# Optimization experiments

Hardware: AMD Instinct MI355X
Metric: run time of the kernel (lower is better)

The kernel has to match this reference:

```python
import jax, jax.numpy as jnp
import numpy as np

H = 256  # rnn_size


def setup_inputs() -> dict:
    key = jax.random.key(0)
    ks = jax.random.split(key, 6)
    B, T, F, D = 64, 512, 64, 64
    s_in = 1.0 / np.sqrt(F)
    s_rec = 1.0 / np.sqrt(H)
    return {
        "x": jax.random.normal(ks[0], (B, T, F), jnp.float32),
        "kernel": jax.random.normal(ks[1], (F, 3 * H), jnp.float32) * s_in,
        "recurrent_kernel": jax.random.normal(ks[2], (H, 3 * H), jnp.float32) * s_rec,
        "bias": jax.random.normal(ks[3], (3 * H,), jnp.float32) * 0.01,
        "dense_w": jax.random.normal(ks[4], (H, D), jnp.float32) * s_rec,
        "dense_b": jax.random.normal(ks[5], (D,), jnp.float32) * 0.01,
    }


def _gru_scan(x, kernel, recurrent_kernel, bias):
    B, T, _ = x.shape
    # Pre-project all timesteps: [B, T, 3H]
    xproj = jnp.einsum("btf,fg->btg", x, kernel) + bias
    xproj_t = jnp.transpose(xproj, (1, 0, 2))  # [T, B, 3H]

    def step(h, xt):
        # Keras GRU, reset_after=False: r gates the recurrent matmul of the candidate
        rec = h @ recurrent_kernel  # [B, 3H]
        xz, xr, xh = xt[:, :H], xt[:, H:2 * H], xt[:, 2 * H:]
        rz, rr, rh = rec[:, :H], rec[:, H:2 * H], rec[:, 2 * H:]
        z = jax.nn.sigmoid(xz + rz)
        r = jax.nn.sigmoid(xr + rr)
        hh = jnp.tanh(xh + r * rh)
        h_new = z * h + (1.0 - z) * hh
        return h_new, h_new

    h0 = jnp.zeros((B, H), x.dtype)
    h_last, outs = jax.lax.scan(step, h0, xproj_t)
    return jnp.transpose(outs, (1, 0, 2)), h_last  # [B,T,H], [B,H]


def reference(x, kernel, recurrent_kernel, bias, dense_w, dense_b):
    outputs, h_last = _gru_scan(x, kernel, recurrent_kernel, bias)
    state = jnp.tanh(h_last @ dense_w + dense_b)  # [B, dense_size]
    return outputs, state
```

## Files before the change

### kernel.cpp

```cpp
#include <hip/hip_runtime.h>


typedef _Float16 half2_t __attribute__((ext_vector_type(2)));
typedef _Float16 f16x4_t __attribute__((ext_vector_type(4)));

#define LOG2E 1.4426950408889634f

__device__ __forceinline__ float fast_sigmoid(float x) {
  float e = __builtin_amdgcn_exp2f(-x * LOG2E);
  return __builtin_amdgcn_rcpf(1.0f + e);
}
__device__ __forceinline__ float fast_tanh(float x) {
  float e = __builtin_amdgcn_exp2f(x * (2.0f * LOG2E));
  return 1.0f - 2.0f * __builtin_amdgcn_rcpf(1.0f + e);
}

__global__ __launch_bounds__(256, 4) void xproj_gemm(
    const float* __restrict__ x, const float* __restrict__ kmat,
    const float* __restrict__ bias, _Float16* __restrict__ xp) {
  __shared__ half2_t As2[32][132];
  __shared__ half2_t Bs2[32][132];
  const int tid = threadIdx.x;
  const int rb = blockIdx.x * 128;
  const int cb = blockIdx.y * 128;

  {
    const int k4 = (tid & 15) * 4;
    const int r0 = tid >> 4;
#pragma unroll
    for (int p = 0; p < 8; ++p) {
      int r = r0 + p * 16;
      float4 v = *(const float4*)(x + (size_t)(rb + r) * 64 + k4);
      half2_t lo, hi;
      lo[0] = (_Float16)v.x; lo[1] = (_Float16)v.y;
      hi[0] = (_Float16)v.z; hi[1] = (_Float16)v.w;
      As2[k4 / 2][r] = lo;
      As2[k4 / 2 + 1][r] = hi;
    }
  }
  {
    const int c4 = (tid & 31) * 4;
    const int kp0 = tid >> 5;
#pragma unroll
    for (int p = 0; p < 4; ++p) {
      int kp = kp0 + p * 8;
      float4 va = *(const float4*)(kmat + (size_t)(2 * kp) * 768 + cb + c4);
      float4 vb = *(const float4*)(kmat + (size_t)(2 * kp + 1) * 768 + cb + c4);
      half2_t o0, o1, o2, o3;
      o0[0] = (_Float16)va.x; o0[1] = (_Float16)vb.x;
      o1[0] = (_Float16)va.y; o1[1] = (_Float16)vb.y;
      o2[0] = (_Float16)va.z; o2[1] = (_Float16)vb.z;
      o3[0] = (_Float16)va.w; o3[1] = (_Float16)vb.w;
      Bs2[kp][c4 + 0] = o0;
      Bs2[kp][c4 + 1] = o1;
      Bs2[kp][c4 + 2] = o2;
      Bs2[kp][c4 + 3] = o3;
    }
  }
  __syncthreads();

  const int tx = tid & 15, ty = tid >> 4;
  const int r0 = ty * 8;
  const int c0 = tx * 4;
  float acc[8][8];
  {
    float4 b0 = *(const float4*)(bias + cb + c0);
    float4 b1 = *(const float4*)(bias + cb + 64 + c0);
    float bz[8] = {b0.x, b0.y, b0.z, b0.w, b1.x, b1.y, b1.z, b1.w};
#pragma unroll
    for (int i = 0; i < 8; ++i)
#pragma unroll
      for (int j = 0; j < 8; ++j) acc[i][j] = bz[j];
  }

#pragma unroll 2
  for (int kp = 0; kp < 32; ++kp) {
    half2_t a2[8], b2[8];
    *(int4*)(&a2[0]) = *(const int4*)(&As2[kp][r0]);
    *(int4*)(&a2[4]) = *(const int4*)(&As2[kp][r0 + 4]);
    *(int2*)(&b2[0]) = *(const int2*)(&Bs2[kp][c0]);
    *(int2*)(&b2[2]) = *(const int2*)(&Bs2[kp][c0 + 2]);
    *(int2*)(&b2[4]) = *(const int2*)(&Bs2[kp][64 + c0]);
    *(int2*)(&b2[6]) = *(const int2*)(&Bs2[kp][64 + c0 + 2]);
#pragma unroll
    for (int i = 0; i < 8; ++i)
#pragma unroll
      for (int j = 0; j < 8; ++j)
        acc[i][j] = __builtin_amdgcn_fdot2(a2[i], b2[j], acc[i][j], false);
  }

#pragma unroll
  for (int i = 0; i < 8; ++i) {
    f16x4_t o0, o1;
#pragma unroll
    for (int j = 0; j < 4; ++j) {
      o0[j] = (_Float16)acc[i][j];
      o1[j] = (_Float16)acc[i][4 + j];
    }
    _Float16* dst = xp + (size_t)(rb + r0 + i) * 768 + cb;
    *(f16x4_t*)(dst + c0) = o0;
    *(f16x4_t*)(dst + 64 + c0) = o1;
  }
}

__global__ __launch_bounds__(512, 2) void gru_scan(
    const _Float16* __restrict__ xp, const float* __restrict__ wr,
    const float* __restrict__ dw, const float* __restrict__ db,
    float* __restrict__ out, float* __restrict__ state) {
  __shared__ float part[3 * 256];
  __shared__ float hbuf[256];
  __shared__ alignas(16) _Float16 hhalf[256];

  const int tid = threadIdx.x;
  const int b = blockIdx.x;
  const int c = tid >> 8;
  const int col = tid & 255;

  half2_t w2[3][64];
#pragma unroll
  for (int q = 0; q < 3; ++q) {
    const float* wp = wr + (size_t)(c * 128) * 768 + col + q * 256;
#pragma unroll
    for (int j = 0; j < 64; ++j) {
      float wa = wp[(size_t)(2 * j) * 768];
      float wb = wp[(size_t)(2 * j + 1) * 768];
      half2_t p;
      p[0] = (_Float16)wa;
      p[1] = (_Float16)wb;
      w2[q][j] = p;
    }
  }

  if (tid < 256) hhalf[tid] = (_Float16)0.0f;
  __syncthreads();

  const _Float16* xpb = xp + (size_t)b * 512 * 768;
  float* outb = out + (size_t)b * 512 * 256;
  const int4* hp = (const int4*)hhalf + c * 16;
  float hprev = 0.0f;

  for (int t = 0; t < 512; ++t) {
    float xz = 0.0f, xr = 0.0f, xh = 0.0f;
    if (tid < 256) {
      const _Float16* xr0 = xpb + (size_t)t * 768 + tid;
      xz = (float)xr0[0];
      xr = (float)xr0[256];
      xh = (float)xr0[512];
    }

    float a0 = 0.0f, a1 = 0.0f, a2 = 0.0f;
    int4 hv = hp[0];
#pragma unroll
    for (int g = 0; g < 16; ++g) {
      int4 hn = hv;
      if (g < 15) hn = hp[g + 1];
      half2_t p0 = __builtin_bit_cast(half2_t, hv.x);
      half2_t p1 = __builtin_bit_cast(half2_t, hv.y);
      half2_t p2 = __builtin_bit_cast(half2_t, hv.z);
      half2_t p3 = __builtin_bit_cast(half2_t, hv.w);
      a0 = __builtin_amdgcn_fdot2(p0, w2[0][g * 4 + 0], a0, false);
      a0 = __builtin_amdgcn_fdot2(p1, w2[0][g * 4 + 1], a0, false);
      a0 = __builtin_amdgcn_fdot2(p2, w2[0][g * 4 + 2], a0, false);
      a0 = __builtin_amdgcn_fdot2(p3, w2[0][g * 4 + 3], a0, false);
      a1 = __builtin_amdgcn_fdot2(p0, w2[1][g * 4 + 0], a1, false);
      a1 = __builtin_amdgcn_fdot2(p1, w2[1][g * 4 + 1], a1, false);
      a1 = __builtin_amdgcn_fdot2(p2, w2[1][g * 4 + 2], a1, false);
      a1 = __builtin_amdgcn_fdot2(p3, w2[1][g * 4 + 3], a1, false);
      a2 = __builtin_amdgcn_fdot2(p0, w2[2][g * 4 + 0], a2, false);
      a2 = __builtin_amdgcn_fdot2(p1, w2[2][g * 4 + 1], a2, false);
      a2 = __builtin_amdgcn_fdot2(p2, w2[2][g * 4 + 2], a2, false);
      a2 = __builtin_amdgcn_fdot2(p3, w2[2][g * 4 + 3], a2, false);
      hv = hn;
    }
    if (tid >= 256) {
      part[col] = a0;
      part[256 + col] = a1;
      part[512 + col] = a2;
    }
    __syncthreads();

    if (tid < 256) {
      const int i = tid;
      if (t) outb[(size_t)(t - 1) * 256 + i] = hprev;
      float rz = a0 + part[i];
      float rr = a1 + part[256 + i];
      float rh = a2 + part[512 + i];
      float z = fast_sigmoid(xz + rz);
      float r = fast_sigmoid(xr + rr);
      float hh = fast_tanh(xh + r * rh);
      float hnew = z * hprev + (1.0f - z) * hh;
      hprev = hnew;
      hhalf[i] = (_Float16)hnew;
    }
    __syncthreads();
  }

  if (tid < 256) {
    outb[(size_t)511 * 256 + tid] = hprev;
    hbuf[tid] = hprev;
  }
  __syncthreads();

  if (tid < 64) {
    float acc = db[tid];
#pragma unroll 8
    for (int k = 0; k < 256; ++k) acc = fmaf(hbuf[k], dw[k * 64 + tid], acc);
    state[(size_t)b * 64 + tid] = fast_tanh(acc);
  }
}

extern "C" void kernel_launch(void* const* d_in, const int* in_sizes, int n_in,
                              void* d_out, int out_size, void* d_ws,
                              size_t ws_size, hipStream_t stream) {
  const float* x = (const float*)d_in[0];
  const float* kmat = (const float*)d_in[1];
  const float* wr = (const float*)d_in[2];
  const float* bias = (const float*)d_in[3];
  const float* dw = (const float*)d_in[4];
  const float* db = (const float*)d_in[5];

  float* out = (float*)d_out;
  float* state = out + (size_t)64 * 512 * 256;
  _Float16* xp = (_Float16*)d_ws;

  dim3 gg(32768 / 128, 768 / 128);
  xproj_gemm<<<gg, 256, 0, stream>>>(x, kmat, bias, xp);
  gru_scan<<<64, 512, 0, stream>>>(xp, wr, dw, db, out, state);
}
```

Baseline: 707.5 us.

## Batch 16 sequences per block and compute GRU recurrence with MFMA

Replaces the per-sequence scan (one block per batch row, fdot2 reductions split over two halves plus a partial-sum exchange) with a block handling 16 batch rows. The recurrent matmul runs as 16x16x32 f16 MFMA with weight fragments held in registers, and h is double-buffered in LDS so each step needs only one barrier. This removes the second barrier and the partial-sum traffic per step and puts the matmul on matrix cores. The trade-off is that only 4 blocks run, so very few CUs are used and each step's latency is bounded by one block's MFMA chain plus scattered xp loads and output stores.

```diff
diff --git a/kernel.cpp b/kernel.cpp
--- a/kernel.cpp
+++ b/kernel.cpp
@@ -3,6 +3,8 @@
 
 typedef _Float16 half2_t __attribute__((ext_vector_type(2)));
 typedef _Float16 f16x4_t __attribute__((ext_vector_type(4)));
+typedef _Float16 f16x8_t __attribute__((ext_vector_type(8)));
+typedef float f32x4_t __attribute__((ext_vector_type(4)));
 
 #define LOG2E 1.4426950408889634f
 
@@ -103,109 +105,99 @@
   }
 }
 
-__global__ __launch_bounds__(512, 2) void gru_scan(
+__global__ __launch_bounds__(512, 1) void gru_scan_mfma(
     const _Float16* __restrict__ xp, const float* __restrict__ wr,
     const float* __restrict__ dw, const float* __restrict__ db,
     float* __restrict__ out, float* __restrict__ state) {
-  __shared__ float part[3 * 256];
-  __shared__ float hbuf[256];
-  __shared__ alignas(16) _Float16 hhalf[256];
+  __shared__ _Float16 hA[2][16][264];
+  __shared__ float hf[16][256];
 
   const int tid = threadIdx.x;
-  const int b = blockIdx.x;
-  const int c = tid >> 8;
-  const int col = tid & 255;
-
-  half2_t w2[3][64];
-#pragma unroll
-  for (int q = 0; q < 3; ++q) {
-    const float* wp = wr + (size_t)(c * 128) * 768 + col + q * 256;
-#pragma unroll
-    for (int j = 0; j < 64; ++j) {
-      float wa = wp[(size_t)(2 * j) * 768];
-      float wb = wp[(size_t)(2 * j + 1) * 768];
-      half2_t p;
-      p[0] = (_Float16)wa;
-      p[1] = (_Float16)wb;
-      w2[q][j] = p;
-    }
-  }
-
-  if (tid < 256) hhalf[tid] = (_Float16)0.0f;
+  const int blk = blockIdx.x;
+  const int w = tid >> 6;
+  const int l = tid & 63;
+  const int q = l >> 4;
+  const int nl = l & 15;
+
+  f16x8_t wfrag[6][8];
+#pragma unroll
+  for (int i = 0; i < 6; ++i) {
+    const int nt = w + 8 * i;
+#pragma unroll
+    for (int kt = 0; kt < 8; ++kt) {
+      f16x8_t f;
+#pragma unroll
+      for (int j = 0; j < 8; ++j)
+        f[j] = (_Float16)wr[(size_t)(kt * 32 + q * 8 + j) * 768 + nt * 16 + nl];
+      wfrag[i][kt] = f;
+    }
+  }
+
+  for (int i = tid; i < 2 * 16 * 264; i += 512) (&hA[0][0][0])[i] = (_Float16)0;
   __syncthreads();
 
-  const _Float16* xpb = xp + (size_t)b * 512 * 768;
-  float* outb = out + (size_t)b * 512 * 256;
-  const int4* hp = (const int4*)hhalf + c * 16;
-  float hprev = 0.0f;
+  float hold[2][4] = {{0.f, 0.f, 0.f, 0.f}, {0.f, 0.f, 0.f, 0.f}};
 
   for (int t = 0; t < 512; ++t) {
-    float xz = 0.0f, xr = 0.0f, xh = 0.0f;
-    if (tid < 256) {
-      const _Float16* xr0 = xpb + (size_t)t * 768 + tid;
-      xz = (float)xr0[0];
-      xr = (float)xr0[256];
-      xh = (float)xr0[512];
-    }
-
-    float a0 = 0.0f, a1 = 0.0f, a2 = 0.0f;
-    int4 hv = hp[0];
-#pragma unroll
-    for (int g = 0; g < 16; ++g) {
-      int4 hn = hv;
-      if (g < 15) hn = hp[g + 1];
-      half2_t p0 = __builtin_bit_cast(half2_t, hv.x);
-      half2_t p1 = __builtin_bit_cast(half2_t, hv.y);
-      half2_t p2 = __builtin_bit_cast(half2_t, hv.z);
-      half2_t p3 = __builtin_bit_cast(half2_t, hv.w);
-      a0 = __builtin_amdgcn_fdot2(p0, w2[0][g * 4 + 0], a0, false);
-      a0 = __builtin_amdgcn_fdot2(p1, w2[0][g * 4 + 1], a0, false);
-      a0 = __builtin_amdgcn_fdot2(p2, w2[0][g * 4 + 2], a0, false);
-      a0 = __builtin_amdgcn_fdot2(p3, w2[0][g * 4 + 3], a0, false);
-      a1 = __builtin_amdgcn_fdot2(p0, w2[1][g * 4 + 0], a1, false);
-      a1 = __builtin_amdgcn_fdot2(p1, w2[1][g * 4 + 1], a1, false);
-      a1 = __builtin_amdgcn_fdot2(p2, w2[1][g * 4 + 2], a1, false);
-      a1 = __builtin_amdgcn_fdot2(p3, w2[1][g * 4 + 3], a1, false);
-      a2 = __builtin_amdgcn_fdot2(p0, w2[2][g * 4 + 0], a2, false);
-      a2 = __builtin_amdgcn_fdot2(p1, w2[2][g * 4 + 1], a2, false);
-      a2 = __builtin_amdgcn_fdot2(p2, w2[2][g * 4 + 2], a2, false);
-      a2 = __builtin_amdgcn_fdot2(p3, w2[2][g * 4 + 3], a2, false);
-      hv = hn;
-    }
-    if (tid >= 256) {
-      part[col] = a0;
-      part[256 + col] = a1;
-      part[512 + col] = a2;
+    const int cur = t & 1;
+
+    _Float16 xzv[2][4], xrv[2][4], xhv[2][4];
+#pragma unroll
+    for (int tr = 0; tr < 2; ++tr) {
+      const int col = (w + 8 * tr) * 16 + nl;
+#pragma unroll
+      for (int r = 0; r < 4; ++r) {
+        const int bm = blk * 16 + q * 4 + r;
+        const _Float16* xrow = xp + ((size_t)bm * 512 + t) * 768;
+        xzv[tr][r] = xrow[col];
+        xrv[tr][r] = xrow[col + 256];
+        xhv[tr][r] = xrow[col + 512];
+      }
+    }
+
+    f32x4_t acc[6];
+#pragma unroll
+    for (int i = 0; i < 6; ++i) acc[i] = (f32x4_t){0.f, 0.f, 0.f, 0.f};
+#pragma unroll
+    for (int kt = 0; kt < 8; ++kt) {
+      f16x8_t afrag = *(const f16x8_t*)&hA[cur][nl][kt * 32 + q * 8];
+#pragma unroll
+      for (int i = 0; i < 6; ++i)
+        acc[i] = __builtin_amdgcn_mfma_f32_16x16x32_f16(afrag, wfrag[i][kt],
+                                                        acc[i], 0, 0, 0);
+    }
+
+#pragma unroll
+    for (int tr = 0; tr < 2; ++tr) {
+      const int col = (w + 8 * tr) * 16 + nl;
+#pragma unroll
+      for (int r = 0; r < 4; ++r) {
+        const int m = q * 4 + r;
+        float z = fast_sigmoid((float)xzv[tr][r] + acc[tr][r]);
+        float rg = fast_sigmoid((float)xrv[tr][r] + acc[2 + tr][r]);
+        float hc = fast_tanh((float)xhv[tr][r] + rg * acc[4 + tr][r]);
+        float hn = z * hold[tr][r] + (1.0f - z) * hc;
+        hold[tr][r] = hn;
+        out[((size_t)(blk * 16 + m) * 512 + t) * 256 + col] = hn;
+        hA[1 - cur][m][col] = (_Float16)hn;
+      }
     }
     __syncthreads();
-
-    if (tid < 256) {
-      const int i = tid;
-      if (t) outb[(size_t)(t - 1) * 256 + i] = hprev;
-      float rz = a0 + part[i];
-      float rr = a1 + part[256 + i];
-      float rh = a2 + part[512 + i];
-      float z = fast_sigmoid(xz + rz);
-      float r = fast_sigmoid(xr + rr);
-      float hh = fast_tanh(xh + r * rh);
-      float hnew = z * hprev + (1.0f - z) * hh;
-      hprev = hnew;
-      hhalf[i] = (_Float16)hnew;
-    }
-    __syncthreads();
-  }
-
-  if (tid < 256) {
-    outb[(size_t)511 * 256 + tid] = hprev;
-    hbuf[tid] = hprev;
-  }
+  }
+
+#pragma unroll
+  for (int tr = 0; tr < 2; ++tr)
+#pragma unroll
+    for (int r = 0; r < 4; ++r)
+      hf[q * 4 + r][(w + 8 * tr) * 16 + nl] = hold[tr][r];
   __syncthreads();
 
-  if (tid < 64) {
-    float acc = db[tid];
+  for (int o = tid; o < 16 * 64; o += 512) {
+    const int m = o >> 6, d = o & 63;
+    float acc = db[d];
 #pragma unroll 8
-    for (int k = 0; k < 256; ++k) acc = fmaf(hbuf[k], dw[k * 64 + tid], acc);
-    state[(size_t)b * 64 + tid] = fast_tanh(acc);
+    for (int k = 0; k < 256; ++k) acc = fmaf(hf[m][k], dw[k * 64 + d], acc);
+    state[(size_t)(blk * 16 + m) * 64 + d] = fast_tanh(acc);
   }
 }
 
@@ -225,5 +217,5 @@
 
   dim3 gg(32768 / 128, 768 / 128);
   xproj_gemm<<<gg, 256, 0, stream>>>(x, kmat, bias, xp);
-  gru_scan<<<64, 512, 0, stream>>>(xp, wr, dw, db, out, state);
-}
+  gru_scan_mfma<<<4, 512, 0, stream>>>(xp, wr, dw, db, out, state);
+}
```

New measurement: 1.524 ms. 2.15x slower.
